# Performance work log

Measured on AMD Instinct MI355X. Metric: run time of the kernel, lower is better.

## Reference

```python
import jax, jax.numpy as jnp
import numpy as np

B, S, H, E = 32, 2048, 1024, 1024
NEG = -10000000000.0


def setup_inputs() -> dict:
    key = jax.random.key(0)
    ks = jax.random.split(key, 8)
    scale = 1.0 / np.sqrt(H)
    return {
        "hidden": jax.random.normal(ks[0], (B, H), jnp.float32),
        "encoder_outputs": jax.random.normal(ks[1], (B, S, E), jnp.float32),
        "mask": jax.random.randint(ks[2], (B, S), 0, 2, jnp.int32),
        "W_h": jax.random.normal(ks[3], (H, H), jnp.float32) * scale,
        "b_h": jax.random.normal(ks[4], (H,), jnp.float32) * scale,
        "W_e": jax.random.normal(ks[5], (E, H), jnp.float32) * scale,
        "b_e": jax.random.normal(ks[6], (H,), jnp.float32) * scale,
        "v": jax.random.normal(ks[7], (H,), jnp.float32) * scale,
    }


def reference(hidden, encoder_outputs, mask, W_h, b_h, W_e, b_e, v):
    # hidden proj: (B,H) -> (B,1,H); encoder proj: (B,S,E) -> (B,S,H)
    h_proj = (hidden @ W_h + b_h)[:, None, :]
    e_proj = jnp.einsum("bse,eh->bsh", encoder_outputs, W_e) + b_e
    energy = jnp.tanh(h_proj + e_proj)                      # (B,S,H)
    attention = jnp.einsum("bsh,h->bs", energy, v)          # (B,S)
    attention = jnp.where(mask == 0, NEG, attention)
    attention_weights = jax.nn.softmax(attention, axis=1)   # (B,S)
    context = jnp.einsum("bs,bse->be", attention_weights, encoder_outputs)
    return (context, attention_weights)
```

## Files before the change

kernel.cpp:

```cpp
#include <hip/hip_runtime.h>

#define NEGV -10000000000.0f

typedef _Float16 half8 __attribute__((ext_vector_type(8)));
typedef float f32x4 __attribute__((ext_vector_type(4)));

__device__ __forceinline__ void gld16(const void* g, void* l) {
  __builtin_amdgcn_global_load_lds((const __attribute__((address_space(1))) void*)g,
                                   (__attribute__((address_space(3))) void*)l,
                                   16, 0, 0);
}

__device__ __forceinline__ float fast_tanh(float x) {
  const float e = __expf(2.0f * x);
  return 1.0f - 2.0f * __builtin_amdgcn_rcpf(e + 1.0f);
}

__global__ __launch_bounds__(256) void prep_kernel(
    const float* __restrict__ We, _Float16* __restrict__ W16T,
    const float* __restrict__ hidden, const float* __restrict__ W_h,
    const float* __restrict__ b_h, const float* __restrict__ b_e,
    float* __restrict__ hpb) {
  __shared__ float tile[32][33];
  const int bid = blockIdx.x;
  const int tid = threadIdx.x;

  if (bid < 128) {
    const int b = bid >> 2;
    const int h = ((bid & 3) << 8) | tid;
    const float* hb = hidden + b * 1024;
    float a0 = 0.f, a1 = 0.f, a2 = 0.f, a3 = 0.f;
    #pragma unroll 4
    for (int k = 0; k < 1024; k += 4) {
      a0 = fmaf(hb[k + 0], W_h[(size_t)(k + 0) * 1024 + h], a0);
      a1 = fmaf(hb[k + 1], W_h[(size_t)(k + 1) * 1024 + h], a1);
      a2 = fmaf(hb[k + 2], W_h[(size_t)(k + 2) * 1024 + h], a2);
      a3 = fmaf(hb[k + 3], W_h[(size_t)(k + 3) * 1024 + h], a3);
    }
    hpb[b * 1024 + h] = b_h[h] + b_e[h] + ((a0 + a1) + (a2 + a3));
  } else {
    const int tb = bid - 128;
    const int n0 = (tb & 31) << 5, k0 = (tb >> 5) << 5;
    const int tx = tid & 31, ty = tid >> 5;
    #pragma unroll
    for (int i = 0; i < 4; ++i) {
      const int r = ty + (i << 3);
      tile[r][tx] = We[(size_t)(k0 + r) * 1024 + n0 + tx];
    }
    __syncthreads();
    #pragma unroll
    for (int i = 0; i < 4; ++i) {
      const int r = ty + (i << 3);
      W16T[(size_t)(n0 + r) * 1024 + k0 + tx] = (_Float16)tile[tx][r];
    }
  }
}

__global__ __launch_bounds__(512, 2) void attn_gemm8_kernel(
    const float* __restrict__ enc32, const _Float16* __restrict__ W16T,
    const float* __restrict__ hpb, const float* __restrict__ v,
    const int* __restrict__ mask, float* __restrict__ logits) {
  __shared__ __align__(16) _Float16 Abuf[3][256 * 32];
  __shared__ __align__(16) _Float16 Bbuf[3][256 * 32];
  __shared__ float hp_s[1024];
  __shared__ float vh_s[1024];
  __shared__ float red[1024];

  const int tid = threadIdx.x;
  const int wid = tid >> 6;
  const int lane = tid & 63;
  const int l15 = lane & 15;
  const int qq = lane >> 4;
  const int wr = wid >> 2;
  const int wc = wid & 3;
  const int m0 = blockIdx.x << 8;
  const int b = blockIdx.x >> 3;

  for (int i = tid; i < 1024; i += 512) {
    hp_s[i] = hpb[(b << 10) + i];
    vh_s[i] = v[i];
  }

  const int r0 = tid >> 2;
  const int r1 = r0 + 128;
  const int g0 = tid & 3;
  const int swzd = (g0 ^ ((r0 >> 1) & 3)) << 4;
  const int scB = swzd;
  const int ldsoff0 = (wid << 10);
  const int ldsoff1 = (wid << 10) + 8192;

  const float* encb = enc32 + (size_t)m0 * 1024;
  const char* wb0 = (const char*)W16T;

  f32x4 af[4];
  auto issueA = [&](int t) {
    const float* p0 = encb + (size_t)r0 * 1024 + ((t & 31) << 5) + (g0 << 3);
    const float* p1 = encb + (size_t)r1 * 1024 + ((t & 31) << 5) + (g0 << 3);
    af[0] = *(const f32x4*)p0; af[1] = *(const f32x4*)(p0 + 4);
    af[2] = *(const f32x4*)p1; af[3] = *(const f32x4*)(p1 + 4);
  };
  auto writeA = [&](int buf) {
    half8 h0, h1;
    #pragma unroll
    for (int j = 0; j < 4; ++j) {
      h0[j] = (_Float16)af[0][j]; h0[4 + j] = (_Float16)af[1][j];
      h1[j] = (_Float16)af[2][j]; h1[4 + j] = (_Float16)af[3][j];
    }
    char* Ab = (char*)(&Abuf[buf][0]);
    *(half8*)(Ab + (r0 << 6) + swzd) = h0;
    *(half8*)(Ab + (r1 << 6) + swzd) = h1;
  };
  auto stageB = [&](int buf, int t) {
    const char* wb = wb0 + ((size_t)(t >> 5) << 19);
    const int colb = ((t & 31) << 6) + scB;
    char* base = (char*)(&Bbuf[buf][0]);
    gld16(wb + (size_t)r0 * 2048 + colb, base + ldsoff0);
    gld16(wb + (size_t)r1 * 2048 + colb, base + ldsoff1);
  };

  int aoff[2][4], boff[4];
  #pragma unroll
  for (int mh = 0; mh < 2; ++mh)
    #pragma unroll
    for (int mi = 0; mi < 4; ++mi) {
      const int row = (wr << 7) + (mh << 6) + (mi << 4) + l15;
      aoff[mh][mi] = (row << 6) + ((qq ^ ((row >> 1) & 3)) << 4);
    }
  #pragma unroll
  for (int ni = 0; ni < 4; ++ni) {
    const int np = (wc << 6) + (ni << 4) + l15;
    boff[ni] = (np << 6) + ((qq ^ ((np >> 1) & 3)) << 4);
  }

  f32x4 acc[8][4];
  float rowsum[8][4];
  #pragma unroll
  for (int mi = 0; mi < 8; ++mi)
    #pragma unroll
    for (int j = 0; j < 4; ++j) {
      acc[mi][j] = (f32x4){0.f, 0.f, 0.f, 0.f};
      rowsum[mi][j] = 0.f;
    }

  issueA(0);
  stageB(0, 0); stageB(1, 1);
  asm volatile("s_waitcnt vmcnt(4)" ::: "memory");
  writeA(0);
  issueA(1);
  __syncthreads();

  #pragma unroll 1
  for (int t = 0; t < 128; ++t) {
    const int bi = t % 3;
    const int bi1 = (bi >= 2) ? 0 : bi + 1;
    const int bi2 = (bi1 >= 2) ? 0 : bi1 + 1;
    const char* A = (const char*)(&Abuf[bi][0]);
    const char* B = (const char*)(&Bbuf[bi][0]);
    half8 a0[4], a1[4], bf[4];

    #pragma unroll
    for (int mi = 0; mi < 4; ++mi) a0[mi] = *(const half8*)(A + aoff[0][mi]);
    #pragma unroll
    for (int ni = 0; ni < 4; ++ni) bf[ni] = *(const half8*)(B + boff[ni]);
    #pragma unroll
    for (int mi = 0; mi < 4; ++mi) a1[mi] = *(const half8*)(A + aoff[1][mi]);

    if (t < 127) writeA(bi1);
    if (t < 126) { issueA(t + 2); stageB(bi2, t + 2); }

    __builtin_amdgcn_s_setprio(1);
    #pragma unroll
    for (int mi = 0; mi < 4; ++mi)
      #pragma unroll
      for (int ni = 0; ni < 4; ++ni)
        acc[mi][ni] = __builtin_amdgcn_mfma_f32_16x16x32_f16(a0[mi], bf[ni], acc[mi][ni], 0, 0, 0);
    #pragma unroll
    for (int mi = 0; mi < 4; ++mi)
      #pragma unroll
      for (int ni = 0; ni < 4; ++ni)
        acc[4 + mi][ni] = __builtin_amdgcn_mfma_f32_16x16x32_f16(a1[mi], bf[ni], acc[4 + mi][ni], 0, 0, 0);
    __builtin_amdgcn_s_setprio(0);

    if (t < 126) asm volatile("s_waitcnt vmcnt(6)" ::: "memory");
    else         asm volatile("s_waitcnt vmcnt(0)" ::: "memory");
    asm volatile("s_waitcnt lgkmcnt(0)" ::: "memory");
    __builtin_amdgcn_s_barrier();

    if ((t & 31) == 31) {
      const int nt = t >> 5;
      const int hb = (nt << 8) + (wc << 6);
      #pragma unroll
      for (int ni = 0; ni < 4; ++ni) {
        const int h = hb + (ni << 4) + l15;
        const float hv = hp_s[h];
        const float vv = vh_s[h];
        #pragma unroll
        for (int mi = 0; mi < 8; ++mi) {
          #pragma unroll
          for (int r = 0; r < 4; ++r)
            rowsum[mi][r] += fast_tanh(acc[mi][ni][r] + hv) * vv;
          acc[mi][ni] = (f32x4){0.f, 0.f, 0.f, 0.f};
        }
      }
    }
  }

  #pragma unroll
  for (int mi = 0; mi < 8; ++mi)
    #pragma unroll
    for (int r = 0; r < 4; ++r) {
      float s = rowsum[mi][r];
      s += __shfl_xor(s, 1);
      s += __shfl_xor(s, 2);
      s += __shfl_xor(s, 4);
      s += __shfl_xor(s, 8);
      rowsum[mi][r] = s;
    }
  __syncthreads();
  if (l15 == 0) {
    #pragma unroll
    for (int mi = 0; mi < 8; ++mi)
      #pragma unroll
      for (int r = 0; r < 4; ++r) {
        const int row = (wr << 7) + (mi << 4) + (qq << 2) + r;
        red[(row << 2) + wc] = rowsum[mi][r];
      }
  }
  __syncthreads();
  if (tid < 256) {
    const float s = red[tid << 2] + red[(tid << 2) + 1] + red[(tid << 2) + 2] + red[(tid << 2) + 3];
    const int m = m0 + tid;
    logits[m] = (mask[(b << 11) + (m & 2047)] == 0) ? NEGV : s;
  }
}

__global__ void softmax_kernel(const float* __restrict__ logits, float* __restrict__ wout) {
  __shared__ float red[4];
  const int b = blockIdx.x, tid = threadIdx.x;
  const int wid = tid >> 6, lane = tid & 63;
  const float* lb = logits + b * 2048;
  float x[8];
  #pragma unroll
  for (int j = 0; j < 8; ++j) x[j] = lb[tid + j * 256];
  float m = x[0];
  #pragma unroll
  for (int j = 1; j < 8; ++j) m = fmaxf(m, x[j]);
  #pragma unroll
  for (int off = 32; off > 0; off >>= 1) m = fmaxf(m, __shfl_xor(m, off));
  if (lane == 0) red[wid] = m;
  __syncthreads();
  m = fmaxf(fmaxf(red[0], red[1]), fmaxf(red[2], red[3]));
  __syncthreads();
  float e[8];
  float s = 0.f;
  #pragma unroll
  for (int j = 0; j < 8; ++j) { e[j] = expf(x[j] - m); s += e[j]; }
  #pragma unroll
  for (int off = 32; off > 0; off >>= 1) s += __shfl_xor(s, off);
  if (lane == 0) red[wid] = s;
  __syncthreads();
  s = red[0] + red[1] + red[2] + red[3];
  const float inv = 1.0f / s;
  #pragma unroll
  for (int j = 0; j < 8; ++j) wout[b * 2048 + tid + j * 256] = e[j] * inv;
}

__global__ void context_kernel(const float* __restrict__ enc, const float* __restrict__ wout,
                               float* __restrict__ ctx) {
  const int b = blockIdx.x >> 4;
  const int ch = blockIdx.x & 15;
  const int tid = threadIdx.x;
  float ax = 0.f, ay = 0.f, az = 0.f, aw = 0.f;
  const int s0 = ch * 128;
  for (int i = 0; i < 128; ++i) {
    const int s = s0 + i;
    const float w = wout[b * 2048 + s];
    const float4 r = *(const float4*)(enc + (size_t)(b * 2048 + s) * 1024 + tid * 4);
    ax = fmaf(w, r.x, ax);
    ay = fmaf(w, r.y, ay);
    az = fmaf(w, r.z, az);
    aw = fmaf(w, r.w, aw);
  }
  float* c = ctx + b * 1024 + tid * 4;
  atomicAdd(c + 0, ax);
  atomicAdd(c + 1, ay);
  atomicAdd(c + 2, az);
  atomicAdd(c + 3, aw);
}

extern "C" void kernel_launch(void* const* d_in, const int* in_sizes, int n_in,
                              void* d_out, int out_size, void* d_ws, size_t ws_size,
                              hipStream_t stream) {
  const float* hidden = (const float*)d_in[0];
  const float* enc    = (const float*)d_in[1];
  const int*   mask   = (const int*)d_in[2];
  const float* W_h    = (const float*)d_in[3];
  const float* b_h    = (const float*)d_in[4];
  const float* W_e    = (const float*)d_in[5];
  const float* b_e    = (const float*)d_in[6];
  const float* v      = (const float*)d_in[7];

  float* ctx  = (float*)d_out;
  float* wout = (float*)d_out + 32 * 1024;

  char* ws = (char*)d_ws;
  _Float16* W16T = (_Float16*)ws;
  float* hpb     = (float*)(ws + 2097152);
  float* logits  = (float*)(ws + 2097152 + 131072);

  hipMemsetAsync(ctx, 0, 32 * 1024 * sizeof(float), stream);
  hipLaunchKernelGGL(prep_kernel, dim3(1152), dim3(256), 0, stream,
                     W_e, W16T, hidden, W_h, b_h, b_e, hpb);
  hipLaunchKernelGGL(attn_gemm8_kernel, dim3(256), dim3(512), 0, stream,
                     enc, W16T, hpb, v, mask, logits);
  hipLaunchKernelGGL(softmax_kernel, dim3(32), dim3(256), 0, stream, logits, wout);
  hipLaunchKernelGGL(context_kernel, dim3(512), dim3(256), 0, stream, enc, wout, ctx);
}
```

Measured before the change: 257.6 us.

## Double K-tile depth to 64 and switch to two-stage buffering

The K tile per iteration grows from 32 to 64, and each iteration runs two MFMA sub-steps, which halves the number of barriers and loop iterations. The triple-buffered LDS ring becomes a double buffer with 128-byte rows and an 8-way XOR swizzle. The next tile's LDS writes and async B loads are now issued between the two MFMA halves. In exchange, prefetch depth drops to one stage for B, the A prefetch needs twice as many registers, and per-iteration VMEM traffic rises, so latency hiding may suffer.

```diff
diff --git a/kernel.cpp b/kernel.cpp
--- a/kernel.cpp
+++ b/kernel.cpp
@@ -60,8 +60,8 @@
     const float* __restrict__ enc32, const _Float16* __restrict__ W16T,
     const float* __restrict__ hpb, const float* __restrict__ v,
     const int* __restrict__ mask, float* __restrict__ logits) {
-  __shared__ __align__(16) _Float16 Abuf[3][256 * 32];
-  __shared__ __align__(16) _Float16 Bbuf[3][256 * 32];
+  __shared__ __align__(16) _Float16 Abuf[2][256 * 64];
+  __shared__ __align__(16) _Float16 Bbuf[2][256 * 64];
   __shared__ float hp_s[1024];
   __shared__ float vh_s[1024];
   __shared__ float red[1024];
@@ -81,55 +81,64 @@
     vh_s[i] = v[i];
   }
 
-  const int r0 = tid >> 2;
-  const int r1 = r0 + 128;
-  const int g0 = tid & 3;
-  const int swzd = (g0 ^ ((r0 >> 1) & 3)) << 4;
-  const int scB = swzd;
-  const int ldsoff0 = (wid << 10);
-  const int ldsoff1 = (wid << 10) + 8192;
+  const int rA = tid >> 3;
+  const int g0 = tid & 7;
+  const int swz = (g0 ^ (rA & 7)) << 4;
+  const int ldsB = (wid << 10);
 
   const float* encb = enc32 + (size_t)m0 * 1024;
   const char* wb0 = (const char*)W16T;
 
-  f32x4 af[4];
+  f32x4 af[8];
   auto issueA = [&](int t) {
-    const float* p0 = encb + (size_t)r0 * 1024 + ((t & 31) << 5) + (g0 << 3);
-    const float* p1 = encb + (size_t)r1 * 1024 + ((t & 31) << 5) + (g0 << 3);
-    af[0] = *(const f32x4*)p0; af[1] = *(const f32x4*)(p0 + 4);
-    af[2] = *(const f32x4*)p1; af[3] = *(const f32x4*)(p1 + 4);
+    #pragma unroll
+    for (int i = 0; i < 4; ++i) {
+      const int row = rA + (i << 6);
+      const float* p = encb + (size_t)row * 1024 + ((t & 15) << 6) + (g0 << 3);
+      af[2 * i] = *(const f32x4*)p;
+      af[2 * i + 1] = *(const f32x4*)(p + 4);
+    }
   };
   auto writeA = [&](int buf) {
-    half8 h0, h1;
-    #pragma unroll
-    for (int j = 0; j < 4; ++j) {
-      h0[j] = (_Float16)af[0][j]; h0[4 + j] = (_Float16)af[1][j];
-      h1[j] = (_Float16)af[2][j]; h1[4 + j] = (_Float16)af[3][j];
-    }
     char* Ab = (char*)(&Abuf[buf][0]);
-    *(half8*)(Ab + (r0 << 6) + swzd) = h0;
-    *(half8*)(Ab + (r1 << 6) + swzd) = h1;
+    #pragma unroll
+    for (int i = 0; i < 4; ++i) {
+      const int row = rA + (i << 6);
+      half8 h;
+      #pragma unroll
+      for (int j = 0; j < 4; ++j) {
+        h[j] = (_Float16)af[2 * i][j];
+        h[4 + j] = (_Float16)af[2 * i + 1][j];
+      }
+      *(half8*)(Ab + (row << 7) + swz) = h;
+    }
   };
   auto stageB = [&](int buf, int t) {
-    const char* wb = wb0 + ((size_t)(t >> 5) << 19);
-    const int colb = ((t & 31) << 6) + scB;
-    char* base = (char*)(&Bbuf[buf][0]);
-    gld16(wb + (size_t)r0 * 2048 + colb, base + ldsoff0);
-    gld16(wb + (size_t)r1 * 2048 + colb, base + ldsoff1);
+    const char* wb = wb0 + ((size_t)(t >> 4) << 19);
+    char* base = (char*)(&Bbuf[buf][0]) + ldsB;
+    #pragma unroll
+    for (int i = 0; i < 4; ++i) {
+      const int row = rA + (i << 6);
+      const int col = ((t & 15) << 7) + swz;
+      gld16(wb + (size_t)row * 2048 + col, base + (i << 13));
+    }
   };
 
-  int aoff[2][4], boff[4];
-  #pragma unroll
-  for (int mh = 0; mh < 2; ++mh)
-    #pragma unroll
-    for (int mi = 0; mi < 4; ++mi) {
-      const int row = (wr << 7) + (mh << 6) + (mi << 4) + l15;
-      aoff[mh][mi] = (row << 6) + ((qq ^ ((row >> 1) & 3)) << 4);
-    }
-  #pragma unroll
-  for (int ni = 0; ni < 4; ++ni) {
-    const int np = (wc << 6) + (ni << 4) + l15;
-    boff[ni] = (np << 6) + ((qq ^ ((np >> 1) & 3)) << 4);
+  int aoff[2][2][4], boff[2][4];
+  #pragma unroll
+  for (int kk = 0; kk < 2; ++kk) {
+    #pragma unroll
+    for (int mh = 0; mh < 2; ++mh)
+      #pragma unroll
+      for (int mi = 0; mi < 4; ++mi) {
+        const int row = (wr << 7) + (mh << 6) + (mi << 4) + l15;
+        aoff[kk][mh][mi] = (row << 7) + ((((kk << 2) + qq) ^ (row & 7)) << 4);
+      }
+    #pragma unroll
+    for (int ni = 0; ni < 4; ++ni) {
+      const int np = (wc << 6) + (ni << 4) + l15;
+      boff[kk][ni] = (np << 7) + ((((kk << 2) + qq) ^ (np & 7)) << 4);
+    }
   }
 
   f32x4 acc[8][4];
@@ -143,51 +152,66 @@
     }
 
   issueA(0);
-  stageB(0, 0); stageB(1, 1);
-  asm volatile("s_waitcnt vmcnt(4)" ::: "memory");
+  asm volatile("s_waitcnt vmcnt(0)" ::: "memory");
   writeA(0);
+  stageB(0, 0);
   issueA(1);
   __syncthreads();
 
   #pragma unroll 1
-  for (int t = 0; t < 128; ++t) {
-    const int bi = t % 3;
-    const int bi1 = (bi >= 2) ? 0 : bi + 1;
-    const int bi2 = (bi1 >= 2) ? 0 : bi1 + 1;
-    const char* A = (const char*)(&Abuf[bi][0]);
-    const char* B = (const char*)(&Bbuf[bi][0]);
-    half8 a0[4], a1[4], bf[4];
-
-    #pragma unroll
-    for (int mi = 0; mi < 4; ++mi) a0[mi] = *(const half8*)(A + aoff[0][mi]);
-    #pragma unroll
-    for (int ni = 0; ni < 4; ++ni) bf[ni] = *(const half8*)(B + boff[ni]);
-    #pragma unroll
-    for (int mi = 0; mi < 4; ++mi) a1[mi] = *(const half8*)(A + aoff[1][mi]);
-
-    if (t < 127) writeA(bi1);
-    if (t < 126) { issueA(t + 2); stageB(bi2, t + 2); }
-
+  for (int t = 0; t < 64; ++t) {
+    const int par = t & 1, npar = par ^ 1;
+    const char* A = (const char*)(&Abuf[par][0]);
+    const char* B = (const char*)(&Bbuf[par][0]);
+    half8 a[2][4], bf[4];
+
+    #pragma unroll
+    for (int mi = 0; mi < 4; ++mi) a[0][mi] = *(const half8*)(A + aoff[0][0][mi]);
+    #pragma unroll
+    for (int ni = 0; ni < 4; ++ni) bf[ni] = *(const half8*)(B + boff[0][ni]);
+    #pragma unroll
+    for (int mi = 0; mi < 4; ++mi) a[1][mi] = *(const half8*)(A + aoff[0][1][mi]);
     __builtin_amdgcn_s_setprio(1);
     #pragma unroll
-    for (int mi = 0; mi < 4; ++mi)
-      #pragma unroll
-      for (int ni = 0; ni < 4; ++ni)
-        acc[mi][ni] = __builtin_amdgcn_mfma_f32_16x16x32_f16(a0[mi], bf[ni], acc[mi][ni], 0, 0, 0);
-    #pragma unroll
-    for (int mi = 0; mi < 4; ++mi)
-      #pragma unroll
-      for (int ni = 0; ni < 4; ++ni)
-        acc[4 + mi][ni] = __builtin_amdgcn_mfma_f32_16x16x32_f16(a1[mi], bf[ni], acc[4 + mi][ni], 0, 0, 0);
+    for (int mh = 0; mh < 2; ++mh)
+      #pragma unroll
+      for (int mi = 0; mi < 4; ++mi)
+        #pragma unroll
+        for (int ni = 0; ni < 4; ++ni)
+          acc[(mh << 2) + mi][ni] =
+              __builtin_amdgcn_mfma_f32_16x16x32_f16(a[mh][mi], bf[ni], acc[(mh << 2) + mi][ni], 0, 0, 0);
     __builtin_amdgcn_s_setprio(0);
 
-    if (t < 126) asm volatile("s_waitcnt vmcnt(6)" ::: "memory");
-    else         asm volatile("s_waitcnt vmcnt(0)" ::: "memory");
+    if (t < 63) {
+      writeA(npar);
+      stageB(npar, t + 1);
+    }
+    if (t < 62) issueA(t + 2);
+
+    #pragma unroll
+    for (int mi = 0; mi < 4; ++mi) a[0][mi] = *(const half8*)(A + aoff[1][0][mi]);
+    #pragma unroll
+    for (int ni = 0; ni < 4; ++ni) bf[ni] = *(const half8*)(B + boff[1][ni]);
+    #pragma unroll
+    for (int mi = 0; mi < 4; ++mi) a[1][mi] = *(const half8*)(A + aoff[1][1][mi]);
+    __builtin_amdgcn_s_setprio(1);
+    #pragma unroll
+    for (int mh = 0; mh < 2; ++mh)
+      #pragma unroll
+      for (int mi = 0; mi < 4; ++mi)
+        #pragma unroll
+        for (int ni = 0; ni < 4; ++ni)
+          acc[(mh << 2) + mi][ni] =
+              __builtin_amdgcn_mfma_f32_16x16x32_f16(a[mh][mi], bf[ni], acc[(mh << 2) + mi][ni], 0, 0, 0);
+    __builtin_amdgcn_s_setprio(0);
+
+    if (t < 62) asm volatile("s_waitcnt vmcnt(8)" ::: "memory");
+    else        asm volatile("s_waitcnt vmcnt(0)" ::: "memory");
     asm volatile("s_waitcnt lgkmcnt(0)" ::: "memory");
     __builtin_amdgcn_s_barrier();
 
-    if ((t & 31) == 31) {
-      const int nt = t >> 5;
+    if ((t & 15) == 15) {
+      const int nt = t >> 4;
       const int hb = (nt << 8) + (wc << 6);
       #pragma unroll
       for (int ni = 0; ni < 4; ++ni) {
```

After: 423.3 us. 1.64x slower.

## Emit fp16 encoder copy from GEMM and read it in context kernel

Applied to the files above, without the earlier changes.

The GEMM kernel already converts encoder outputs to fp16 for its A tiles. During the first N-tile pass it now also stores those converted tiles to a workspace buffer. The context kernel then reads this fp16 copy, which halves its read traffic compared with re-reading the fp32 input. In exchange the GEMM writes an extra 128 MB, its vmcnt waits are adjusted to account for the pending stores, and the context result is accumulated from fp16-rounded inputs.

```diff
diff --git a/kernel.cpp b/kernel.cpp
--- a/kernel.cpp
+++ b/kernel.cpp
@@ -57,7 +57,8 @@
 }
 
 __global__ __launch_bounds__(512, 2) void attn_gemm8_kernel(
-    const float* __restrict__ enc32, const _Float16* __restrict__ W16T,
+    const float* __restrict__ enc32, _Float16* __restrict__ enc16,
+    const _Float16* __restrict__ W16T,
     const float* __restrict__ hpb, const float* __restrict__ v,
     const int* __restrict__ mask, float* __restrict__ logits) {
   __shared__ __align__(16) _Float16 Abuf[3][256 * 32];
@@ -90,6 +91,7 @@
   const int ldsoff1 = (wid << 10) + 8192;
 
   const float* encb = enc32 + (size_t)m0 * 1024;
+  _Float16* enc16b = enc16 + (size_t)m0 * 1024;
   const char* wb0 = (const char*)W16T;
 
   f32x4 af[4];
@@ -99,7 +101,7 @@
     af[0] = *(const f32x4*)p0; af[1] = *(const f32x4*)(p0 + 4);
     af[2] = *(const f32x4*)p1; af[3] = *(const f32x4*)(p1 + 4);
   };
-  auto writeA = [&](int buf) {
+  auto writeA = [&](int buf, int t1) {
     half8 h0, h1;
     #pragma unroll
     for (int j = 0; j < 4; ++j) {
@@ -109,6 +111,11 @@
     char* Ab = (char*)(&Abuf[buf][0]);
     *(half8*)(Ab + (r0 << 6) + swzd) = h0;
     *(half8*)(Ab + (r1 << 6) + swzd) = h1;
+    if (t1 >= 1 && t1 <= 32) {
+      const int kc = ((t1 & 31) << 5) + (g0 << 3);
+      *(half8*)(enc16b + (size_t)r0 * 1024 + kc) = h0;
+      *(half8*)(enc16b + (size_t)r1 * 1024 + kc) = h1;
+    }
   };
   auto stageB = [&](int buf, int t) {
     const char* wb = wb0 + ((size_t)(t >> 5) << 19);
@@ -145,7 +152,7 @@
   issueA(0);
   stageB(0, 0); stageB(1, 1);
   asm volatile("s_waitcnt vmcnt(4)" ::: "memory");
-  writeA(0);
+  writeA(0, 0);
   issueA(1);
   __syncthreads();
 
@@ -165,7 +172,7 @@
     #pragma unroll
     for (int mi = 0; mi < 4; ++mi) a1[mi] = *(const half8*)(A + aoff[1][mi]);
 
-    if (t < 127) writeA(bi1);
+    if (t < 127) writeA(bi1, t + 1);
     if (t < 126) { issueA(t + 2); stageB(bi2, t + 2); }
 
     __builtin_amdgcn_s_setprio(1);
@@ -181,8 +188,9 @@
         acc[4 + mi][ni] = __builtin_amdgcn_mfma_f32_16x16x32_f16(a1[mi], bf[ni], acc[4 + mi][ni], 0, 0, 0);
     __builtin_amdgcn_s_setprio(0);
 
-    if (t < 126) asm volatile("s_waitcnt vmcnt(6)" ::: "memory");
-    else         asm volatile("s_waitcnt vmcnt(0)" ::: "memory");
+    if (t < 32)       asm volatile("s_waitcnt vmcnt(8)" ::: "memory");
+    else if (t < 126) asm volatile("s_waitcnt vmcnt(6)" ::: "memory");
+    else              asm volatile("s_waitcnt vmcnt(0)" ::: "memory");
     asm volatile("s_waitcnt lgkmcnt(0)" ::: "memory");
     __builtin_amdgcn_s_barrier();
 
@@ -265,27 +273,24 @@
   for (int j = 0; j < 8; ++j) wout[b * 2048 + tid + j * 256] = e[j] * inv;
 }
 
-__global__ void context_kernel(const float* __restrict__ enc, const float* __restrict__ wout,
-                               float* __restrict__ ctx) {
+__global__ void context16_kernel(const _Float16* __restrict__ enc16,
+                                 const float* __restrict__ wout, float* __restrict__ ctx) {
   const int b = blockIdx.x >> 4;
   const int ch = blockIdx.x & 15;
-  const int tid = threadIdx.x;
-  float ax = 0.f, ay = 0.f, az = 0.f, aw = 0.f;
-  const int s0 = ch * 128;
-  for (int i = 0; i < 128; ++i) {
-    const int s = s0 + i;
-    const float w = wout[b * 2048 + s];
-    const float4 r = *(const float4*)(enc + (size_t)(b * 2048 + s) * 1024 + tid * 4);
-    ax = fmaf(w, r.x, ax);
-    ay = fmaf(w, r.y, ay);
-    az = fmaf(w, r.z, az);
-    aw = fmaf(w, r.w, aw);
-  }
-  float* c = ctx + b * 1024 + tid * 4;
-  atomicAdd(c + 0, ax);
-  atomicAdd(c + 1, ay);
-  atomicAdd(c + 2, az);
-  atomicAdd(c + 3, aw);
+  const int tl = threadIdx.x & 127;
+  const int sh = threadIdx.x >> 7;
+  float a[8] = {0.f, 0.f, 0.f, 0.f, 0.f, 0.f, 0.f, 0.f};
+  #pragma unroll 1
+  for (int i = 0; i < 64; ++i) {
+    const int s = (ch << 7) + (i << 1) + sh;
+    const float w = wout[(b << 11) + s];
+    const half8 r = *(const half8*)(enc16 + (((size_t)(b << 11) + s) << 10) + (tl << 3));
+    #pragma unroll
+    for (int j = 0; j < 8; ++j) a[j] = fmaf(w, (float)r[j], a[j]);
+  }
+  float* c = ctx + (b << 10) + (tl << 3);
+  #pragma unroll
+  for (int j = 0; j < 8; ++j) atomicAdd(c + j, a[j]);
 }
 
 extern "C" void kernel_launch(void* const* d_in, const int* in_sizes, int n_in,
@@ -304,15 +309,17 @@
   float* wout = (float*)d_out + 32 * 1024;
 
   char* ws = (char*)d_ws;
-  _Float16* W16T = (_Float16*)ws;
-  float* hpb     = (float*)(ws + 2097152);
-  float* logits  = (float*)(ws + 2097152 + 131072);
+  const size_t ENC16_BYTES = 134217728ULL;
+  _Float16* enc16 = (_Float16*)ws;
+  _Float16* W16T  = (_Float16*)(ws + ENC16_BYTES);
+  float* hpb      = (float*)(ws + ENC16_BYTES + 2097152);
+  float* logits   = (float*)(ws + ENC16_BYTES + 2097152 + 131072);
 
   hipMemsetAsync(ctx, 0, 32 * 1024 * sizeof(float), stream);
   hipLaunchKernelGGL(prep_kernel, dim3(1152), dim3(256), 0, stream,
                      W_e, W16T, hidden, W_h, b_h, b_e, hpb);
   hipLaunchKernelGGL(attn_gemm8_kernel, dim3(256), dim3(512), 0, stream,
-                     enc, W16T, hpb, v, mask, logits);
+                     enc, enc16, W16T, hpb, v, mask, logits);
   hipLaunchKernelGGL(softmax_kernel, dim3(32), dim3(256), 0, stream, logits, wout);
-  hipLaunchKernelGGL(context_kernel, dim3(512), dim3(256), 0, stream, enc, wout, ctx);
-}
+  hipLaunchKernelGGL(context16_kernel, dim3(512), dim3(256), 0, stream, enc16, wout, ctx);
+}
```

Measured after the change: 386.4 us. +50.0%, slower.
